# Kernel optimization log

Measured on AMD Instinct MI355X. Metric: run time of the kernel, lower is better.

## Reference

```python
import jax, jax.numpy as jnp
import numpy as np

B, L, C = 4, 2048, 1024
H = 16
D = C // H  # 64
MAX_SCALE_MUL = float(np.log(100.0))


def setup_inputs() -> dict:
    key = jax.random.key(0)
    ks = jax.random.split(key, 8)
    x = jax.random.normal(ks[0], (B, L, C), dtype=jnp.float32)
    attn_bias = jax.random.normal(ks[1], (1, H, L, L), dtype=jnp.float32) * 0.02
    # nn.Linear(C, 3C, bias=False): weight [3C, C], init ~ U(-1/sqrt(C), 1/sqrt(C))
    lim = 1.0 / np.sqrt(C)
    W_qkv = jax.random.uniform(ks[2], (3 * C, C), minval=-lim, maxval=lim, dtype=jnp.float32)
    q_bias = jnp.zeros((C,), dtype=jnp.float32)
    v_bias = jnp.zeros((C,), dtype=jnp.float32)
    scale_mul_log = jnp.full((1, H, 1, 1), np.log(4.0), dtype=jnp.float32)
    W_proj = jax.random.uniform(ks[3], (C, C), minval=-lim, maxval=lim, dtype=jnp.float32)
    b_proj = jax.random.uniform(ks[4], (C,), minval=-lim, maxval=lim, dtype=jnp.float32)
    return {"x": x, "attn_bias": attn_bias, "W_qkv": W_qkv, "q_bias": q_bias,
            "v_bias": v_bias, "scale_mul_log": scale_mul_log,
            "W_proj": W_proj, "b_proj": b_proj}


def reference(x, attn_bias, W_qkv, q_bias, v_bias, scale_mul_log, W_proj, b_proj):
    Bc, Lc, Cc = x.shape
    qkv_bias = jnp.concatenate([q_bias, jnp.zeros_like(q_bias), v_bias])
    qkv = x @ W_qkv.T + qkv_bias                      # [B, L, 3C]
    qkv = qkv.reshape(Bc, Lc, 3, H, D)
    q, k, v = jnp.moveaxis(qkv, 2, 0)                 # each [B, L, H, D]
    q = jnp.swapaxes(q, 1, 2)                         # [B, H, L, D]
    k = jnp.swapaxes(k, 1, 2)
    v = jnp.swapaxes(v, 1, 2)
    # L2-norm cosine attention with learned per-head scale
    scale_mul = jnp.exp(jnp.minimum(scale_mul_log, MAX_SCALE_MUL))  # [1, H, 1, 1]
    q = q / jnp.linalg.norm(q, axis=-1, keepdims=True).clip(1e-12) * scale_mul
    k = k / jnp.linalg.norm(k, axis=-1, keepdims=True).clip(1e-12)
    attn = jnp.einsum('bhqd,bhkd->bhqk', q, k) + attn_bias
    attn = jax.nn.softmax(attn, axis=-1)
    out = jnp.einsum('bhqk,bhkd->bhqd', attn, v)      # [B, H, L, D]
    out = jnp.swapaxes(out, 1, 2).reshape(Bc, Lc, Cc)
    return out @ W_proj.T + b_proj
```

## Files before the change

### kernel.cpp

```cpp
#include <hip/hip_runtime.h>
#include <cstdint>
#include <cstddef>

#define BATCH 4
#define SEQ   2048
#define CMOD  1024
#define NH    16
#define DH    64
#define LOG100 4.6051701859880914f
#define LOG2E  1.4426950408889634f

typedef __attribute__((ext_vector_type(8))) short bf16x8;
typedef __attribute__((ext_vector_type(4))) float f32x4;

__device__ __forceinline__ float bf2f(uint16_t u) {
    union { uint32_t i; float f; } x; x.i = ((uint32_t)u) << 16; return x.f;
}
__device__ __forceinline__ uint16_t f2bf(float f) {
    union { float f; uint32_t i; } x; x.f = f;
    uint32_t u = x.i;
    return (uint16_t)((u + 0x7FFFu + ((u >> 16) & 1u)) >> 16);
}
__device__ __forceinline__ float exp2_fast(float x) {
    float r; asm("v_exp_f32 %0, %1" : "=v"(r) : "v"(x)); return r;
}

__device__ __forceinline__ void gload_lds16(const void* g, void* l) {
    __builtin_amdgcn_global_load_lds(
        (const __attribute__((address_space(1))) uint32_t*)g,
        (__attribute__((address_space(3))) uint32_t*)l,
        16, 0, 0);
}

__global__ __launch_bounds__(256) void cvt_kernel(const float* __restrict__ in,
                                                  uint16_t* __restrict__ out, int n) {
    int i = (blockIdx.x * 256 + threadIdx.x) * 4;
    if (i >= n) return;
    float4 f = *(const float4*)(in + i);
    ushort4 o;
    o.x = f2bf(f.x); o.y = f2bf(f.y); o.z = f2bf(f.z); o.w = f2bf(f.w);
    *(ushort4*)(out + i) = o;
}

__global__ __launch_bounds__(256) void gemm_bt_kernel(
    const uint16_t* __restrict__ A, const uint16_t* __restrict__ B,
    int M, int N, int K, int mode,
    uint16_t* __restrict__ qb, uint16_t* __restrict__ kb, uint16_t* __restrict__ vtb,
    const float* __restrict__ q_bias, const float* __restrict__ v_bias,
    const float* __restrict__ scale_mul_log,
    float* __restrict__ outp, const float* __restrict__ b_proj)
{
    __shared__ __align__(16) uint16_t As[128 * 32];
    __shared__ __align__(16) uint16_t Bs[128 * 32];
    const int t = threadIdx.x;
    const int wave = t >> 6, lane = t & 63;
    const int g = lane >> 4, c16 = lane & 15;
    const int m0 = blockIdx.x * 128, n0 = blockIdx.y * 128;
    const int wm = (wave >> 1) * 64, wn = (wave & 1) * 64;

    f32x4 acc[4][4];
#pragma unroll
    for (int mt = 0; mt < 4; mt++)
#pragma unroll
        for (int nt = 0; nt < 4; nt++) acc[mt][nt] = (f32x4){0.f, 0.f, 0.f, 0.f};

    for (int k0 = 0; k0 < K; k0 += 32) {
        __syncthreads();
#pragma unroll
        for (int i = 0; i < 2; i++) {
            int cc = i * 256 + t;
            int row = cc >> 2, col = (cc & 3) * 8;
            gload_lds16(A + (size_t)(m0 + row) * K + k0 + col, &As[cc * 8]);
            gload_lds16(B + (size_t)(n0 + row) * K + k0 + col, &Bs[cc * 8]);
        }
        __syncthreads();
        bf16x8 af[4], bfv[4];
#pragma unroll
        for (int mt = 0; mt < 4; mt++)
            af[mt] = *(const bf16x8*)&As[(wm + mt * 16 + c16) * 32 + g * 8];
#pragma unroll
        for (int nt = 0; nt < 4; nt++)
            bfv[nt] = *(const bf16x8*)&Bs[(wn + nt * 16 + c16) * 32 + g * 8];
#pragma unroll
        for (int mt = 0; mt < 4; mt++)
#pragma unroll
            for (int nt = 0; nt < 4; nt++)
                acc[mt][nt] = __builtin_amdgcn_mfma_f32_16x16x32_bf16(af[mt], bfv[nt], acc[mt][nt], 0, 0, 0);
    }

    if (mode == 0) {
        const int colbase = n0 + wn;
        const int tt = colbase >> 10;
        const int cc0 = colbase & 1023;
        const int hh = cc0 >> 6;
        float qmul = 1.0f;
        if (tt == 0) qmul = __expf(fminf(scale_mul_log[hh], LOG100)) * LOG2E;
#pragma unroll
        for (int mt = 0; mt < 4; mt++) {
            float vals[4][4];
            float n2[4] = {0.f, 0.f, 0.f, 0.f};
#pragma unroll
            for (int nt = 0; nt < 4; nt++) {
                const int ci = cc0 + nt * 16 + c16;
                float badd = 0.f;
                if (tt == 0) badd = q_bias[ci];
                else if (tt == 2) badd = v_bias[ci];
#pragma unroll
                for (int r = 0; r < 4; r++) {
                    float v = acc[mt][nt][r] + badd;
                    vals[nt][r] = v;
                    n2[r] += v * v;
                }
            }
            float rs[4];
            if (tt < 2) {
#pragma unroll
                for (int r = 0; r < 4; r++) {
                    float s = n2[r];
                    s += __shfl_xor(s, 1, 64);
                    s += __shfl_xor(s, 2, 64);
                    s += __shfl_xor(s, 4, 64);
                    s += __shfl_xor(s, 8, 64);
                    rs[r] = qmul / fmaxf(sqrtf(s), 1e-12f);
                }
            } else {
#pragma unroll
                for (int r = 0; r < 4; r++) rs[r] = 1.0f;
            }
#pragma unroll
            for (int nt = 0; nt < 4; nt++) {
                const int dd = (cc0 + nt * 16 + c16) & 63;
#pragma unroll
                for (int r = 0; r < 4; r++) {
                    const int row = m0 + wm + mt * 16 + g * 4 + r;
                    const int bb = row >> 11, ll = row & 2047;
                    const size_t bhx = (size_t)bb * NH + hh;
                    const uint16_t val = f2bf(vals[nt][r] * rs[r]);
                    if (tt == 0)      qb[(bhx * SEQ + ll) * DH + dd] = val;
                    else if (tt == 1) kb[(bhx * SEQ + ll) * DH + dd] = val;
                    else              vtb[(bhx * DH + dd) * SEQ + ll] = val;
                }
            }
        }
    } else {
#pragma unroll
        for (int mt = 0; mt < 4; mt++)
#pragma unroll
            for (int nt = 0; nt < 4; nt++)
#pragma unroll
                for (int r = 0; r < 4; r++) {
                    int row = m0 + wm + mt * 16 + g * 4 + r;
                    int col = n0 + wn + nt * 16 + c16;
                    outp[(size_t)row * N + col] = acc[mt][nt][r] + b_proj[col];
                }
    }
}

__global__ __launch_bounds__(256) void attn_kernel(
    const uint16_t* __restrict__ qb, const uint16_t* __restrict__ kb,
    const uint16_t* __restrict__ vtb, const float* __restrict__ bias,
    uint16_t* __restrict__ ob)
{
    __shared__ __align__(16) uint16_t Ks[4][64 * 64];
    __shared__ __align__(16) uint16_t Vs[4][64 * 64];
    __shared__ __align__(16) uint16_t Ps[4][32 * 64];

    const int t = threadIdx.x;
    const int w = t >> 6, lane = t & 63;
    const int g = lane >> 4, c16 = lane & 15;

    const int h = blockIdx.x >> 6;
    const int qt = blockIdx.x & 63;
    const int q0 = qt * 32;
    const size_t bh = (size_t)w * NH + h;

    bf16x8 qf[2][2];
#pragma unroll
    for (int mt = 0; mt < 2; mt++) {
        const uint16_t* qp = qb + (bh * SEQ + q0 + mt * 16 + c16) * DH + g * 8;
        qf[mt][0] = *(const bf16x8*)(qp);
        qf[mt][1] = *(const bf16x8*)(qp + 32);
    }

    f32x4 accO[2][4];
    float lrun[2][4];
#pragma unroll
    for (int mt = 0; mt < 2; mt++)
#pragma unroll
        for (int nt = 0; nt < 4; nt++) accO[mt][nt] = (f32x4){0.f, 0.f, 0.f, 0.f};
#pragma unroll
    for (int mt = 0; mt < 2; mt++)
#pragma unroll
        for (int r = 0; r < 4; r++) lrun[mt][r] = 0.f;

    const float* bias_base = bias + ((size_t)h * SEQ + q0) * SEQ;

    for (int k0 = 0; k0 < SEQ; k0 += 64) {
        __syncthreads();
#pragma unroll
        for (int i = 0; i < 8; i++) {
            int c = i * 256 + t;
            int bw = c >> 9, cc = c & 511;
            int row = cc >> 3, jc = cc & 7, sj = jc ^ (row & 7);
            gload_lds16(kb + (((size_t)bw * NH + h) * SEQ + k0 + row) * DH + sj * 8, &Ks[bw][cc * 8]);
            gload_lds16(vtb + (((size_t)bw * NH + h) * DH + row) * SEQ + k0 + sj * 8, &Vs[bw][cc * 8]);
        }
        float bb[2][4][4];
#pragma unroll
        for (int mt = 0; mt < 2; mt++)
#pragma unroll
            for (int r = 0; r < 4; r++) {
                const float* bp = bias_base + (size_t)(mt * 16 + g * 4 + r) * SEQ + k0 + c16;
#pragma unroll
                for (int nt = 0; nt < 4; nt++) bb[mt][r][nt] = bp[nt * 16];
            }
        __syncthreads();

        f32x4 S[2][4];
#pragma unroll
        for (int mt = 0; mt < 2; mt++)
#pragma unroll
            for (int nt = 0; nt < 4; nt++) S[mt][nt] = (f32x4){0.f, 0.f, 0.f, 0.f};
#pragma unroll
        for (int kk = 0; kk < 2; kk++) {
            bf16x8 bk[4];
#pragma unroll
            for (int nt = 0; nt < 4; nt++) {
                int rr = nt * 16 + c16;
                bk[nt] = *(const bf16x8*)((const uint8_t*)Ks[w] + rr * 128 + ((kk * 64 + g * 16) ^ ((rr & 7) << 4)));
            }
#pragma unroll
            for (int mt = 0; mt < 2; mt++)
#pragma unroll
                for (int nt = 0; nt < 4; nt++)
                    S[mt][nt] = __builtin_amdgcn_mfma_f32_16x16x32_bf16(qf[mt][kk], bk[nt], S[mt][nt], 0, 0, 0);
        }

#pragma unroll
        for (int mt = 0; mt < 2; mt++)
#pragma unroll
            for (int r = 0; r < 4; r++) {
                const int prow = mt * 16 + g * 4 + r;
                float lp = 0.f;
#pragma unroll
                for (int nt = 0; nt < 4; nt++) {
                    float p = exp2_fast(fmaf(bb[mt][r][nt], LOG2E, S[mt][nt][r]));
                    lp += p;
                    int col = nt * 16 + c16;
                    *(uint16_t*)((uint8_t*)Ps[w] + prow * 128 + ((col * 2) ^ ((prow & 7) << 4))) = f2bf(p);
                }
                lrun[mt][r] += lp;
            }

#pragma unroll
        for (int kk = 0; kk < 2; kk++) {
            bf16x8 pa[2];
#pragma unroll
            for (int mt = 0; mt < 2; mt++)
                pa[mt] = *(const bf16x8*)((const uint8_t*)Ps[w] + (mt * 16 + c16) * 128 + ((kk * 64 + g * 16) ^ ((c16 & 7) << 4)));
#pragma unroll
            for (int nt = 0; nt < 4; nt++) {
                int d = nt * 16 + c16;
                bf16x8 vv = *(const bf16x8*)((const uint8_t*)Vs[w] + d * 128 + ((kk * 64 + g * 16) ^ ((d & 7) << 4)));
#pragma unroll
                for (int mt = 0; mt < 2; mt++)
                    accO[mt][nt] = __builtin_amdgcn_mfma_f32_16x16x32_bf16(pa[mt], vv, accO[mt][nt], 0, 0, 0);
            }
        }
    }

    float linv[2][4];
#pragma unroll
    for (int mt = 0; mt < 2; mt++)
#pragma unroll
        for (int r = 0; r < 4; r++) {
            float s = lrun[mt][r];
            s += __shfl_xor(s, 1, 64);
            s += __shfl_xor(s, 2, 64);
            s += __shfl_xor(s, 4, 64);
            s += __shfl_xor(s, 8, 64);
            linv[mt][r] = 1.0f / s;
        }
#pragma unroll
    for (int mt = 0; mt < 2; mt++)
#pragma unroll
        for (int nt = 0; nt < 4; nt++)
#pragma unroll
            for (int r = 0; r < 4; r++) {
                int qr = q0 + mt * 16 + g * 4 + r;
                int col = h * DH + nt * 16 + c16;
                ob[((size_t)w * SEQ + qr) * CMOD + col] = f2bf(accO[mt][nt][r] * linv[mt][r]);
            }
}

extern "C" void kernel_launch(void* const* d_in, const int* in_sizes, int n_in,
                              void* d_out, int out_size, void* d_ws, size_t ws_size,
                              hipStream_t stream) {
    const float* x             = (const float*)d_in[0];
    const float* attn_bias     = (const float*)d_in[1];
    const float* W_qkv         = (const float*)d_in[2];
    const float* q_bias        = (const float*)d_in[3];
    const float* v_bias        = (const float*)d_in[4];
    const float* scale_mul_log = (const float*)d_in[5];
    const float* W_proj        = (const float*)d_in[6];
    const float* b_proj        = (const float*)d_in[7];
    float* out = (float*)d_out;

    uint8_t* ws = (uint8_t*)d_ws;
    size_t off = 0;
    auto alloc = [&](size_t bytes) { uint8_t* p = ws + off; off += (bytes + 255) & ~(size_t)255; return p; };
    uint16_t* xb     = (uint16_t*)alloc((size_t)8192 * 1024 * 2);
    uint16_t* wqkvb  = (uint16_t*)alloc((size_t)3072 * 1024 * 2);
    uint16_t* wprojb = (uint16_t*)alloc((size_t)1024 * 1024 * 2);
    uint16_t* qb     = (uint16_t*)alloc((size_t)BATCH * NH * SEQ * DH * 2);
    uint16_t* kb     = (uint16_t*)alloc((size_t)BATCH * NH * SEQ * DH * 2);
    uint16_t* vtb    = (uint16_t*)alloc((size_t)BATCH * NH * SEQ * DH * 2);
    uint16_t* ob     = (uint16_t*)alloc((size_t)BATCH * SEQ * CMOD * 2);
    (void)ws_size;

    cvt_kernel<<<8192, 256, 0, stream>>>(x, xb, 8388608);
    cvt_kernel<<<3072, 256, 0, stream>>>(W_qkv, wqkvb, 3145728);
    cvt_kernel<<<1024, 256, 0, stream>>>(W_proj, wprojb, 1048576);

    dim3 g1(64, 24);
    gemm_bt_kernel<<<g1, 256, 0, stream>>>(xb, wqkvb, 8192, 3072, 1024, 0,
                                           qb, kb, vtb, q_bias, v_bias, scale_mul_log,
                                           nullptr, nullptr);

    attn_kernel<<<1024, 256, 0, stream>>>(qb, kb, vtb, attn_bias, ob);

    dim3 g3(64, 8);
    gemm_bt_kernel<<<g3, 256, 0, stream>>>(ob, wprojb, 8192, 1024, 1024, 1,
                                           nullptr, nullptr, nullptr, nullptr, nullptr, nullptr,
                                           out, b_proj);
}
```

Measured before the change: 345.4 us.

## Use 32x32 MFMA with transposed S and register-resident P via permlane swap

Rewrites the attention inner loop to use 32x32x16 bf16 MFMA and computes S transposed (K as the A operand), so each lane owns one query row. The probabilities are packed to bf16 with v_cvt_pk_bf16 and rearranged with permlane32_swap directly into the A-operand layout for the PV MFMA. This removes the LDS round trip for P and its swizzled scalar stores, and turns the bias loads into float4 row reads. The trade-offs are more register pressure from the 16-wide accumulators and reliance on gfx950-specific permlane instructions.

```diff
diff --git a/kernel.cpp b/kernel.cpp
--- a/kernel.cpp
+++ b/kernel.cpp
@@ -12,6 +12,7 @@
 
 typedef __attribute__((ext_vector_type(8))) short bf16x8;
 typedef __attribute__((ext_vector_type(4))) float f32x4;
+typedef __attribute__((ext_vector_type(16))) float f32x16;
 
 __device__ __forceinline__ float bf2f(uint16_t u) {
     union { uint32_t i; float f; } x; x.i = ((uint32_t)u) << 16; return x.f;
@@ -23,6 +24,19 @@
 }
 __device__ __forceinline__ float exp2_fast(float x) {
     float r; asm("v_exp_f32 %0, %1" : "=v"(r) : "v"(x)); return r;
+}
+__device__ __forceinline__ uint32_t cvt_pk_bf16(float lo, float hi) {
+    uint32_t r;
+    asm("v_cvt_pk_bf16_f32 %0, %1, %2" : "=v"(r) : "v"(lo), "v"(hi));
+    return r;
+}
+__device__ __forceinline__ void p32swap(uint32_t& x, uint32_t& y) {
+#if __has_builtin(__builtin_amdgcn_permlane32_swap)
+    auto r = __builtin_amdgcn_permlane32_swap(x, y, false, false);
+    x = r[0]; y = r[1];
+#else
+    asm volatile("v_permlane32_swap_b32 %0, %1\n\ts_nop 1" : "+v"(x), "+v"(y));
+#endif
 }
 
 __device__ __forceinline__ void gload_lds16(const void* g, void* l) {
@@ -163,37 +177,30 @@
 {
     __shared__ __align__(16) uint16_t Ks[4][64 * 64];
     __shared__ __align__(16) uint16_t Vs[4][64 * 64];
-    __shared__ __align__(16) uint16_t Ps[4][32 * 64];
 
     const int t = threadIdx.x;
     const int w = t >> 6, lane = t & 63;
-    const int g = lane >> 4, c16 = lane & 15;
+    const int c32 = lane & 31, hi = lane >> 5;
 
     const int h = blockIdx.x >> 6;
     const int qt = blockIdx.x & 63;
     const int q0 = qt * 32;
     const size_t bh = (size_t)w * NH + h;
 
-    bf16x8 qf[2][2];
-#pragma unroll
-    for (int mt = 0; mt < 2; mt++) {
-        const uint16_t* qp = qb + (bh * SEQ + q0 + mt * 16 + c16) * DH + g * 8;
-        qf[mt][0] = *(const bf16x8*)(qp);
-        qf[mt][1] = *(const bf16x8*)(qp + 32);
-    }
-
-    f32x4 accO[2][4];
-    float lrun[2][4];
-#pragma unroll
-    for (int mt = 0; mt < 2; mt++)
-#pragma unroll
-        for (int nt = 0; nt < 4; nt++) accO[mt][nt] = (f32x4){0.f, 0.f, 0.f, 0.f};
-#pragma unroll
-    for (int mt = 0; mt < 2; mt++)
-#pragma unroll
-        for (int r = 0; r < 4; r++) lrun[mt][r] = 0.f;
-
-    const float* bias_base = bias + ((size_t)h * SEQ + q0) * SEQ;
+    bf16x8 qf[4];
+    const uint16_t* qp = qb + (bh * SEQ + q0 + c32) * DH;
+#pragma unroll
+    for (int s = 0; s < 4; s++)
+        qf[s] = *(const bf16x8*)(qp + s * 16 + hi * 8);
+
+    f32x16 accO[2];
+#pragma unroll
+    for (int db = 0; db < 2; db++)
+#pragma unroll
+        for (int i = 0; i < 16; i++) accO[db][i] = 0.f;
+    float lrun = 0.f;
+
+    const float* bias_base = bias + ((size_t)h * SEQ + q0 + c32) * SEQ;
 
     for (int k0 = 0; k0 < SEQ; k0 += 64) {
         __syncthreads();
@@ -205,92 +212,86 @@
             gload_lds16(kb + (((size_t)bw * NH + h) * SEQ + k0 + row) * DH + sj * 8, &Ks[bw][cc * 8]);
             gload_lds16(vtb + (((size_t)bw * NH + h) * DH + row) * SEQ + k0 + sj * 8, &Vs[bw][cc * 8]);
         }
-        float bb[2][4][4];
-#pragma unroll
-        for (int mt = 0; mt < 2; mt++)
-#pragma unroll
-            for (int r = 0; r < 4; r++) {
-                const float* bp = bias_base + (size_t)(mt * 16 + g * 4 + r) * SEQ + k0 + c16;
-#pragma unroll
-                for (int nt = 0; nt < 4; nt++) bb[mt][r][nt] = bp[nt * 16];
+        float bbf[2][16];
+#pragma unroll
+        for (int kb2 = 0; kb2 < 2; kb2++)
+#pragma unroll
+            for (int tt = 0; tt < 4; tt++) {
+                float4 v4 = *(const float4*)(bias_base + k0 + kb2 * 32 + tt * 8 + hi * 4);
+                bbf[kb2][tt * 4 + 0] = v4.x;
+                bbf[kb2][tt * 4 + 1] = v4.y;
+                bbf[kb2][tt * 4 + 2] = v4.z;
+                bbf[kb2][tt * 4 + 3] = v4.w;
             }
         __syncthreads();
 
-        f32x4 S[2][4];
-#pragma unroll
-        for (int mt = 0; mt < 2; mt++)
-#pragma unroll
-            for (int nt = 0; nt < 4; nt++) S[mt][nt] = (f32x4){0.f, 0.f, 0.f, 0.f};
-#pragma unroll
-        for (int kk = 0; kk < 2; kk++) {
-            bf16x8 bk[4];
-#pragma unroll
-            for (int nt = 0; nt < 4; nt++) {
-                int rr = nt * 16 + c16;
-                bk[nt] = *(const bf16x8*)((const uint8_t*)Ks[w] + rr * 128 + ((kk * 64 + g * 16) ^ ((rr & 7) << 4)));
-            }
-#pragma unroll
-            for (int mt = 0; mt < 2; mt++)
-#pragma unroll
-                for (int nt = 0; nt < 4; nt++)
-                    S[mt][nt] = __builtin_amdgcn_mfma_f32_16x16x32_bf16(qf[mt][kk], bk[nt], S[mt][nt], 0, 0, 0);
-        }
-
-#pragma unroll
-        for (int mt = 0; mt < 2; mt++)
-#pragma unroll
-            for (int r = 0; r < 4; r++) {
-                const int prow = mt * 16 + g * 4 + r;
-                float lp = 0.f;
-#pragma unroll
-                for (int nt = 0; nt < 4; nt++) {
-                    float p = exp2_fast(fmaf(bb[mt][r][nt], LOG2E, S[mt][nt][r]));
-                    lp += p;
-                    int col = nt * 16 + c16;
-                    *(uint16_t*)((uint8_t*)Ps[w] + prow * 128 + ((col * 2) ^ ((prow & 7) << 4))) = f2bf(p);
-                }
-                lrun[mt][r] += lp;
-            }
-
-#pragma unroll
-        for (int kk = 0; kk < 2; kk++) {
-            bf16x8 pa[2];
-#pragma unroll
-            for (int mt = 0; mt < 2; mt++)
-                pa[mt] = *(const bf16x8*)((const uint8_t*)Ps[w] + (mt * 16 + c16) * 128 + ((kk * 64 + g * 16) ^ ((c16 & 7) << 4)));
-#pragma unroll
-            for (int nt = 0; nt < 4; nt++) {
-                int d = nt * 16 + c16;
-                bf16x8 vv = *(const bf16x8*)((const uint8_t*)Vs[w] + d * 128 + ((kk * 64 + g * 16) ^ ((d & 7) << 4)));
-#pragma unroll
-                for (int mt = 0; mt < 2; mt++)
-                    accO[mt][nt] = __builtin_amdgcn_mfma_f32_16x16x32_bf16(pa[mt], vv, accO[mt][nt], 0, 0, 0);
+        f32x16 S[2];
+#pragma unroll
+        for (int kb2 = 0; kb2 < 2; kb2++)
+#pragma unroll
+            for (int i = 0; i < 16; i++) S[kb2][i] = 0.f;
+#pragma unroll
+        for (int s = 0; s < 4; s++) {
+#pragma unroll
+            for (int kb2 = 0; kb2 < 2; kb2++) {
+                int rr = kb2 * 32 + c32;
+                bf16x8 kf = *(const bf16x8*)((const uint8_t*)Ks[w] + rr * 128 +
+                                             (((2 * s + hi) * 16) ^ ((rr & 7) << 4)));
+                S[kb2] = __builtin_amdgcn_mfma_f32_32x32x16_bf16(kf, qf[s], S[kb2], 0, 0, 0);
+            }
+        }
+
+        bf16x8 pa[4];
+#pragma unroll
+        for (int kb2 = 0; kb2 < 2; kb2++) {
+            float p[16];
+            float lp = 0.f;
+#pragma unroll
+            for (int r = 0; r < 16; r++) {
+                p[r] = exp2_fast(fmaf(bbf[kb2][r], LOG2E, S[kb2][r]));
+                lp += p[r];
+            }
+            lrun += lp;
+#pragma unroll
+            for (int cp = 0; cp < 2; cp++) {
+                uint32_t X0 = cvt_pk_bf16(p[8 * cp + 0], p[8 * cp + 1]);
+                uint32_t X1 = cvt_pk_bf16(p[8 * cp + 2], p[8 * cp + 3]);
+                uint32_t Y0 = cvt_pk_bf16(p[8 * cp + 4], p[8 * cp + 5]);
+                uint32_t Y1 = cvt_pk_bf16(p[8 * cp + 6], p[8 * cp + 7]);
+                p32swap(X0, Y0);
+                p32swap(X1, Y1);
+                union { uint32_t u[4]; bf16x8 v; } pu;
+                pu.u[0] = X0; pu.u[1] = X1; pu.u[2] = Y0; pu.u[3] = Y1;
+                pa[kb2 * 2 + cp] = pu.v;
+            }
+        }
+
+#pragma unroll
+        for (int c = 0; c < 4; c++) {
+#pragma unroll
+            for (int db = 0; db < 2; db++) {
+                int rr = db * 32 + c32;
+                bf16x8 vf = *(const bf16x8*)((const uint8_t*)Vs[w] + rr * 128 +
+                                             (((2 * c + hi) * 16) ^ ((rr & 7) << 4)));
+                accO[db] = __builtin_amdgcn_mfma_f32_32x32x16_bf16(pa[c], vf, accO[db], 0, 0, 0);
             }
         }
     }
 
-    float linv[2][4];
-#pragma unroll
-    for (int mt = 0; mt < 2; mt++)
-#pragma unroll
-        for (int r = 0; r < 4; r++) {
-            float s = lrun[mt][r];
-            s += __shfl_xor(s, 1, 64);
-            s += __shfl_xor(s, 2, 64);
-            s += __shfl_xor(s, 4, 64);
-            s += __shfl_xor(s, 8, 64);
-            linv[mt][r] = 1.0f / s;
-        }
-#pragma unroll
-    for (int mt = 0; mt < 2; mt++)
-#pragma unroll
-        for (int nt = 0; nt < 4; nt++)
-#pragma unroll
-            for (int r = 0; r < 4; r++) {
-                int qr = q0 + mt * 16 + g * 4 + r;
-                int col = h * DH + nt * 16 + c16;
-                ob[((size_t)w * SEQ + qr) * CMOD + col] = f2bf(accO[mt][nt][r] * linv[mt][r]);
-            }
+    float ssum = lrun + __shfl_xor(lrun, 32, 64);
+    float inv = 1.0f / ssum;
+    float linv[16];
+#pragma unroll
+    for (int r = 0; r < 16; r++)
+        linv[r] = __shfl(inv, (r & 3) + 8 * (r >> 2) + 4 * hi, 64);
+#pragma unroll
+    for (int db = 0; db < 2; db++)
+#pragma unroll
+        for (int r = 0; r < 16; r++) {
+            int rowq = (r & 3) + 8 * (r >> 2) + 4 * hi;
+            ob[((size_t)w * SEQ + q0 + rowq) * CMOD + h * DH + db * 32 + c32] =
+                f2bf(accO[db][r] * linv[r]);
+        }
 }
 
 extern "C" void kernel_launch(void* const* d_in, const int* in_sizes, int n_in,
```

After: 383.2 us. 1.11x slower.
